# Optimization experiments

Hardware: AMD Instinct MI355X
Metric: run time of the kernel (lower is better)

## Reference

```python
import jax, jax.numpy as jnp
import numpy as np

D_MODEL = 1024
N_HEADS = 16
D_HEAD = D_MODEL // N_HEADS


def setup_inputs() -> dict:
    key = jax.random.key(0)
    k_x, k_qkv, k_out = jax.random.split(key, 3)
    x = jax.random.normal(k_x, (2, 2048, D_MODEL), dtype=jnp.float32)
    # nn.Linear weights: out = x @ W.T ; store as [out_features, in_features]
    s = 1.0 / np.sqrt(D_MODEL)
    w_qkv = jax.random.uniform(k_qkv, (3 * D_MODEL, D_MODEL), jnp.float32, -s, s)
    w_out = jax.random.uniform(k_out, (D_MODEL, D_MODEL), jnp.float32, -s, s)
    return {"x": x, "w_qkv": w_qkv, "w_out": w_out}


def reference(x, w_qkv, w_out):
    B, T, D = x.shape
    qkv = jnp.einsum("btd,ed->bte", x, w_qkv)  # [B,T,3D]
    q, k, v = jnp.split(qkv, 3, axis=-1)

    def heads(t):  # [B,T,D] -> [B,H,T,d]
        return t.reshape(B, T, N_HEADS, D_HEAD).transpose(0, 2, 1, 3)

    q, k, v = heads(q), heads(k), heads(v)
    scale = jnp.float32(np.sqrt(D_HEAD))
    scores = jnp.einsum("bhqd,bhkd->bhqk", q, k) / scale  # [B,H,T,T]
    causal = jnp.tril(jnp.ones((T, T), dtype=bool))  # True = keep
    scores = jnp.where(causal, scores, -jnp.inf)
    attn = jax.nn.softmax(scores, axis=-1)
    out = jnp.einsum("bhqk,bhkd->bhqd", attn, v)
    out = out.transpose(0, 2, 1, 3).reshape(B, T, D)
    return jnp.einsum("btd,ed->bte", out, w_out)
```

## Files before the change

### kernel.cpp

```cpp
#include <hip/hip_runtime.h>
#include <hip/hip_bf16.h>

typedef __attribute__((ext_vector_type(8))) short bf16x8;
typedef __attribute__((ext_vector_type(8))) unsigned short ushort8;
typedef __attribute__((ext_vector_type(4))) float f32x4;
typedef __attribute__((ext_vector_type(16))) float f32x16;

typedef const __attribute__((address_space(1))) void gvoid;
typedef __attribute__((address_space(3))) void svoid;

__device__ __forceinline__ unsigned short f2bf(float f) {
  union { float f; unsigned int u; } v; v.f = f;
  unsigned int u = v.u;
  unsigned int r = (u + 0x7fffu + ((u >> 16) & 1u)) >> 16;
  return (unsigned short)r;
}

__global__ void cast3_kernel(const float* __restrict__ a, int na4,
                             const float* __restrict__ b, int nb4,
                             const float* __restrict__ c, int nc4,
                             unsigned short* __restrict__ oa,
                             unsigned short* __restrict__ ob,
                             unsigned short* __restrict__ oc) {
  const int total = na4 + nb4 + nc4;
  for (int i = blockIdx.x * 256 + threadIdx.x; i < total; i += gridDim.x * 256) {
    const float* src; unsigned short* dst; int j = i;
    if (j < na4) { src = a; dst = oa; }
    else if (j < na4 + nb4) { j -= na4; src = b; dst = ob; }
    else { j -= na4 + nb4; src = c; dst = oc; }
    const float4 v = reinterpret_cast<const float4*>(src)[j];
    ushort4 o4;
    o4.x = f2bf(v.x); o4.y = f2bf(v.y); o4.z = f2bf(v.z); o4.w = f2bf(v.w);
    reinterpret_cast<ushort4*>(dst)[j] = o4;
  }
}

template<bool OUT_BF16>
__global__ __launch_bounds__(256) void gemm_bt(const unsigned short* __restrict__ A,
                                               const unsigned short* __restrict__ B,
                                               void* __restrict__ Cv,
                                               int M, int N, int K,
                                               float qscale, int qcols) {
  constexpr int BM = 128, BK = 32, TILE = BM * BK;
  __shared__ alignas(16) unsigned short As[2 * TILE];
  __shared__ alignas(16) unsigned short Bs[2 * TILE];
  const int tid = threadIdx.x;
  const int l  = tid & 63;
  const int w  = tid >> 6;
  const int wr = w >> 1, wc = w & 1;
  const int lr = l & 15, lg = l >> 4;
  const long tile_m = (long)blockIdx.x * BM;
  const long tile_n = (long)blockIdx.y * BM;

  const int c0 = tid, c1 = tid + 256;
  const unsigned short* pa0 = A + (tile_m + (c0 >> 2)) * (long)K + (c0 & 3) * 8;
  const unsigned short* pa1 = A + (tile_m + (c1 >> 2)) * (long)K + (c1 & 3) * 8;
  const unsigned short* pb0 = B + (tile_n + (c0 >> 2)) * (long)K + (c0 & 3) * 8;
  const unsigned short* pb1 = B + (tile_n + (c1 >> 2)) * (long)K + (c1 & 3) * 8;
  const int woff = w * 512;

  f32x4 acc[4][4] = {};

  __builtin_amdgcn_global_load_lds((gvoid*)pa0, (svoid*)(As + woff), 16, 0, 0);
  __builtin_amdgcn_global_load_lds((gvoid*)pa1, (svoid*)(As + 2048 + woff), 16, 0, 0);
  __builtin_amdgcn_global_load_lds((gvoid*)pb0, (svoid*)(Bs + woff), 16, 0, 0);
  __builtin_amdgcn_global_load_lds((gvoid*)pb1, (svoid*)(Bs + 2048 + woff), 16, 0, 0);
  __syncthreads();

  int cur = 0;
  for (int k0 = 0; k0 < K; k0 += BK) {
    if (k0 + BK < K) {
      unsigned short* An = As + (cur ^ 1) * TILE;
      unsigned short* Bn = Bs + (cur ^ 1) * TILE;
      __builtin_amdgcn_global_load_lds((gvoid*)(pa0 + k0 + BK), (svoid*)(An + woff), 16, 0, 0);
      __builtin_amdgcn_global_load_lds((gvoid*)(pa1 + k0 + BK), (svoid*)(An + 2048 + woff), 16, 0, 0);
      __builtin_amdgcn_global_load_lds((gvoid*)(pb0 + k0 + BK), (svoid*)(Bn + woff), 16, 0, 0);
      __builtin_amdgcn_global_load_lds((gvoid*)(pb1 + k0 + BK), (svoid*)(Bn + 2048 + woff), 16, 0, 0);
    }
    const unsigned short* AsC = As + cur * TILE;
    const unsigned short* BsC = Bs + cur * TILE;
    bf16x8 af[4], bfr[4];
#pragma unroll
    for (int m = 0; m < 4; ++m)
      af[m] = *reinterpret_cast<const bf16x8*>(AsC + (wr * 64 + m * 16 + lr) * BK + lg * 8);
#pragma unroll
    for (int n = 0; n < 4; ++n)
      bfr[n] = *reinterpret_cast<const bf16x8*>(BsC + (wc * 64 + n * 16 + lr) * BK + lg * 8);
#pragma unroll
    for (int m = 0; m < 4; ++m)
#pragma unroll
      for (int n = 0; n < 4; ++n)
        acc[m][n] = __builtin_amdgcn_mfma_f32_16x16x32_bf16(af[m], bfr[n], acc[m][n], 0, 0, 0);
    __syncthreads();
    cur ^= 1;
  }

#pragma unroll
  for (int m = 0; m < 4; ++m)
#pragma unroll
    for (int n = 0; n < 4; ++n)
#pragma unroll
      for (int r = 0; r < 4; ++r) {
        long row = tile_m + wr * 64 + m * 16 + lg * 4 + r;
        long col = tile_n + wc * 64 + n * 16 + lr;
        float sc = (col < qcols) ? qscale : 1.0f;
        if (OUT_BF16)
          reinterpret_cast<unsigned short*>(Cv)[row * N + col] = f2bf(acc[m][n][r] * sc);
        else
          reinterpret_cast<float*>(Cv)[row * N + col] = acc[m][n][r] * sc;
      }
}

__global__ __launch_bounds__(256, 2) void attn_kernel(const unsigned short* __restrict__ qkv,
                                                      unsigned short* __restrict__ o) {
  constexpr int E = 3072, T = 2048;
  __shared__ alignas(16) unsigned short Ks[64 * 64];
  __shared__ alignas(16) unsigned short Vt[64 * 64];
  __shared__ float alBuf[4][32];
  const int tid = threadIdx.x;
  const int l = tid & 63, w = tid >> 6;
  const int hh = l >> 5;
  const int lc = l & 31;
  const int id = blockIdx.x;
  const int half = id >> 8, rr2 = id & 255;
  const int bx = rr2 & 15;
  const int bh = (rr2 >> 4) | (half << 4);
  const int qtb = half ? (15 - bx) : bx;
  const int b = bh >> 4, hd = bh & 15;
  const unsigned short* Qb = qkv + (size_t)b * T * E + hd * 64;
  const unsigned short* Kb = Qb + 1024;
  const unsigned short* Vb = Qb + 2048;

  const int qrow0 = qtb * 128 + w * 32;
  const int qg = qrow0 + lc;
  const int nt = 2 * qtb + 2;

  const int kr0 = tid >> 3, js0 = tid & 7;
  const int kr1 = kr0 + 32;
  const unsigned short* sK = Kb + (size_t)kr0 * E + js0 * 8;
  const unsigned short* sV = Vb + (size_t)kr0 * E + js0 * 8;
  const size_t tileStep = (size_t)64 * E;

  bf16x8 aq[4];
#pragma unroll
  for (int c = 0; c < 4; ++c)
    aq[c] = *reinterpret_cast<const bf16x8*>(Qb + (size_t)qg * E + c * 16 + hh * 8);

  f32x16 accO0 = {}, accO1 = {};
  float mL = -1e30f, ls = 0.f;

  ushort8 k0 = *reinterpret_cast<const ushort8*>(sK);
  ushort8 k1 = *reinterpret_cast<const ushort8*>(sK + 32 * E);
  ushort8 v0 = *reinterpret_cast<const ushort8*>(sV);
  ushort8 v1 = *reinterpret_cast<const ushort8*>(sV + 32 * E);

  for (int t = 0; t < nt; ++t) {
    __syncthreads();
    *reinterpret_cast<ushort8*>(Ks + kr0 * 64 + ((js0 ^ (kr0 & 7)) << 3)) = k0;
    *reinterpret_cast<ushort8*>(Ks + kr1 * 64 + ((js0 ^ (kr1 & 7)) << 3)) = k1;
#pragma unroll
    for (int e = 0; e < 8; ++e) {
      int d = js0 * 8 + e;
      int swz = (d ^ (d >> 3)) & 7;
      Vt[d * 64 + ((((kr0 >> 3) ^ swz) << 3) | (kr0 & 7))] = (unsigned short)v0[e];
      Vt[d * 64 + ((((kr1 >> 3) ^ swz) << 3) | (kr1 & 7))] = (unsigned short)v1[e];
    }
    __syncthreads();
    if (t + 1 < nt) {
      const unsigned short* nK = sK + (size_t)(t + 1) * tileStep;
      const unsigned short* nV = sV + (size_t)(t + 1) * tileStep;
      k0 = *reinterpret_cast<const ushort8*>(nK);
      k1 = *reinterpret_cast<const ushort8*>(nK + 32 * E);
      v0 = *reinterpret_cast<const ushort8*>(nV);
      v1 = *reinterpret_cast<const ushort8*>(nV + 32 * E);
    }

    if (t * 64 > qrow0 + 31) continue;

    f32x16 sT0 = {}, sT1 = {};
#pragma unroll
    for (int c = 0; c < 4; ++c) {
      int sl = ((2 * c + hh) ^ (lc & 7)) << 3;
      bf16x8 ak0 = *reinterpret_cast<const bf16x8*>(Ks + lc * 64 + sl);
      bf16x8 ak1 = *reinterpret_cast<const bf16x8*>(Ks + (32 + lc) * 64 + sl);
      sT0 = __builtin_amdgcn_mfma_f32_32x32x16_bf16(ak0, aq[c], sT0, 0, 0, 0);
      sT1 = __builtin_amdgcn_mfma_f32_32x32x16_bf16(ak1, aq[c], sT1, 0, 0, 0);
    }

    const bool needMask = (t * 64 + 63) > qrow0;
    float pm = -1e30f;
#pragma unroll
    for (int r = 0; r < 16; ++r) {
      int kb = t * 64 + (r & 3) + 8 * (r >> 2) + 4 * hh;
      float a0 = sT0[r], a1 = sT1[r];
      if (needMask) {
        if (kb > qg) a0 = -1e30f;
        if (kb + 32 > qg) a1 = -1e30f;
      }
      sT0[r] = a0; sT1[r] = a1;
      pm = fmaxf(pm, fmaxf(a0, a1));
    }
    pm = fmaxf(pm, __shfl_xor(pm, 32));

    if (__any(pm > mL + 8.f)) {
      float mn = fmaxf(mL, pm);
      float al = __expf(mL - mn);
      mL = mn;
      ls *= al;
      alBuf[w][lc] = al;
      asm volatile("s_waitcnt lgkmcnt(0)" ::: "memory");
      __builtin_amdgcn_sched_barrier(0);
#pragma unroll
      for (int r = 0; r < 16; ++r) {
        float alr = alBuf[w][(r & 3) + 8 * (r >> 2) + 4 * hh];
        accO0[r] *= alr;
        accO1[r] *= alr;
      }
    }

    bf16x8 pa[4];
    union U4 { unsigned int u[4]; bf16x8 v; };
#pragma unroll
    for (int n = 0; n < 2; ++n) {
      float p[16];
#pragma unroll
      for (int r = 0; r < 16; ++r) {
        float pv = __expf((n ? sT1[r] : sT0[r]) - mL);
        p[r] = pv;
        ls += pv;
      }
#pragma unroll
      for (int gg = 0; gg < 2; ++gg) {
        unsigned int x0, x1, y0, y1;
        asm("v_cvt_pk_bf16_f32 %0, %1, %2" : "=v"(x0) : "v"(p[8 * gg + 0]), "v"(p[8 * gg + 1]));
        asm("v_cvt_pk_bf16_f32 %0, %1, %2" : "=v"(x1) : "v"(p[8 * gg + 2]), "v"(p[8 * gg + 3]));
        asm("v_cvt_pk_bf16_f32 %0, %1, %2" : "=v"(y0) : "v"(p[8 * gg + 4]), "v"(p[8 * gg + 5]));
        asm("v_cvt_pk_bf16_f32 %0, %1, %2" : "=v"(y1) : "v"(p[8 * gg + 6]), "v"(p[8 * gg + 7]));
        asm("v_permlane32_swap_b32 %0, %1" : "+v"(x0), "+v"(y0));
        asm("v_permlane32_swap_b32 %0, %1" : "+v"(x1), "+v"(y1));
        U4 fu;
        fu.u[0] = x0; fu.u[1] = x1; fu.u[2] = y0; fu.u[3] = y1;
        pa[2 * n + gg] = fu.v;
      }
    }

#pragma unroll
    for (int cp = 0; cp < 4; ++cp) {
      int d0 = lc, d1 = 32 + lc;
      int sl0 = ((2 * cp + hh) ^ ((d0 ^ (d0 >> 3)) & 7)) << 3;
      int sl1 = ((2 * cp + hh) ^ ((d1 ^ (d1 >> 3)) & 7)) << 3;
      bf16x8 bv0 = *reinterpret_cast<const bf16x8*>(Vt + d0 * 64 + sl0);
      bf16x8 bv1 = *reinterpret_cast<const bf16x8*>(Vt + d1 * 64 + sl1);
      accO0 = __builtin_amdgcn_mfma_f32_32x32x16_bf16(pa[cp], bv0, accO0, 0, 0, 0);
      accO1 = __builtin_amdgcn_mfma_f32_32x32x16_bf16(pa[cp], bv1, accO1, 0, 0, 0);
    }
  }

  float inv = 1.f / (ls + __shfl_xor(ls, 32));
  alBuf[w][lc] = inv;
  asm volatile("s_waitcnt lgkmcnt(0)" ::: "memory");
  __builtin_amdgcn_sched_barrier(0);
#pragma unroll
  for (int r = 0; r < 16; ++r) {
    int q = (r & 3) + 8 * (r >> 2) + 4 * hh;
    float iv = alBuf[w][q];
    size_t row = (size_t)(b * T + qrow0 + q) * 1024 + hd * 64;
    o[row + lc]      = f2bf(accO0[r] * iv);
    o[row + 32 + lc] = f2bf(accO1[r] * iv);
  }
}

extern "C" void kernel_launch(void* const* d_in, const int* in_sizes, int n_in,
                              void* d_out, int out_size, void* d_ws, size_t ws_size,
                              hipStream_t stream) {
  const float* x     = (const float*)d_in[0];
  const float* w_qkv = (const float*)d_in[1];
  const float* w_out = (const float*)d_in[2];
  float* out = (float*)d_out;

  unsigned short* xb    = (unsigned short*)d_ws;
  unsigned short* wqkvb = xb    + (size_t)4096 * 1024;
  unsigned short* woutb = wqkvb + (size_t)3072 * 1024;
  unsigned short* qkv   = woutb + (size_t)1024 * 1024;
  unsigned short* attn  = qkv   + (size_t)4096 * 3072;

  cast3_kernel<<<dim3(2048), 256, 0, stream>>>(x,     4096 * 1024 / 4,
                                               w_qkv, 3072 * 1024 / 4,
                                               w_out, 1024 * 1024 / 4,
                                               xb, wqkvb, woutb);

  gemm_bt<true ><<<dim3(32, 24), 256, 0, stream>>>(xb,   wqkvb, (void*)qkv,  4096, 3072, 1024,
                                                   0.125f, 1024);
  attn_kernel  <<<dim3(512), 256, 0, stream>>>(qkv, attn);
  gemm_bt<false><<<dim3(32,  8), 256, 0, stream>>>(attn, woutb, (void*)out, 4096, 1024, 1024,
                                                   1.0f, 0);
}
```

Baseline: 116.8 us.

## Split attention key tiles across two wave groups and merge softmax partials

The attention block grows to 512 threads. Each pair of waves shares the same 32 query rows, and each wave handles one 32-key half of every 64-key tile with its own running max and sum. At the end the two partial outputs are combined through shared memory with a log-sum-exp rescale. This aims to double the waves per block so more latency can be hidden, and it halves per-wave score work and register pressure. In exchange it adds shared memory for the merge, an extra reduction phase, and a larger workgroup that may fit fewer blocks per CU.

```diff
diff --git a/kernel.cpp b/kernel.cpp
--- a/kernel.cpp
+++ b/kernel.cpp
@@ -111,16 +111,20 @@
       }
 }
 
-__global__ __launch_bounds__(256, 2) void attn_kernel(const unsigned short* __restrict__ qkv,
+__global__ __launch_bounds__(512, 2) void attn_kernel(const unsigned short* __restrict__ qkv,
                                                       unsigned short* __restrict__ o) {
   constexpr int E = 3072, T = 2048;
   __shared__ alignas(16) unsigned short Ks[64 * 64];
   __shared__ alignas(16) unsigned short Vt[64 * 64];
-  __shared__ float alBuf[4][32];
+  __shared__ float OB[4][32][64];
+  __shared__ float alBuf[8][32];
+  __shared__ float mB[4][32], lB[4][32], fA[4][32], fB[4][32];
   const int tid = threadIdx.x;
   const int l = tid & 63, w = tid >> 6;
   const int hh = l >> 5;
   const int lc = l & 31;
+  const int wq = w & 3;
+  const int h2 = w >> 2;
   const int id = blockIdx.x;
   const int half = id >> 8, rr2 = id & 255;
   const int bx = rr2 & 15;
@@ -131,14 +135,13 @@
   const unsigned short* Kb = Qb + 1024;
   const unsigned short* Vb = Qb + 2048;
 
-  const int qrow0 = qtb * 128 + w * 32;
+  const int qrow0 = qtb * 128 + wq * 32;
   const int qg = qrow0 + lc;
   const int nt = 2 * qtb + 2;
 
-  const int kr0 = tid >> 3, js0 = tid & 7;
-  const int kr1 = kr0 + 32;
-  const unsigned short* sK = Kb + (size_t)kr0 * E + js0 * 8;
-  const unsigned short* sV = Vb + (size_t)kr0 * E + js0 * 8;
+  const int kr = tid >> 3, js = tid & 7;
+  const unsigned short* sK = Kb + (size_t)kr * E + js * 8;
+  const unsigned short* sV = Vb + (size_t)kr * E + js * 8;
   const size_t tileStep = (size_t)64 * E;
 
   bf16x8 aq[4];
@@ -150,55 +153,43 @@
   float mL = -1e30f, ls = 0.f;
 
   ushort8 k0 = *reinterpret_cast<const ushort8*>(sK);
-  ushort8 k1 = *reinterpret_cast<const ushort8*>(sK + 32 * E);
   ushort8 v0 = *reinterpret_cast<const ushort8*>(sV);
-  ushort8 v1 = *reinterpret_cast<const ushort8*>(sV + 32 * E);
+  const int ksl = (js ^ (kr & 7)) << 3;
 
   for (int t = 0; t < nt; ++t) {
     __syncthreads();
-    *reinterpret_cast<ushort8*>(Ks + kr0 * 64 + ((js0 ^ (kr0 & 7)) << 3)) = k0;
-    *reinterpret_cast<ushort8*>(Ks + kr1 * 64 + ((js0 ^ (kr1 & 7)) << 3)) = k1;
+    *reinterpret_cast<ushort8*>(Ks + kr * 64 + ksl) = k0;
 #pragma unroll
     for (int e = 0; e < 8; ++e) {
-      int d = js0 * 8 + e;
+      int d = js * 8 + e;
       int swz = (d ^ (d >> 3)) & 7;
-      Vt[d * 64 + ((((kr0 >> 3) ^ swz) << 3) | (kr0 & 7))] = (unsigned short)v0[e];
-      Vt[d * 64 + ((((kr1 >> 3) ^ swz) << 3) | (kr1 & 7))] = (unsigned short)v1[e];
+      Vt[d * 64 + ((((kr >> 3) ^ swz) << 3) | (kr & 7))] = (unsigned short)v0[e];
     }
     __syncthreads();
     if (t + 1 < nt) {
-      const unsigned short* nK = sK + (size_t)(t + 1) * tileStep;
-      const unsigned short* nV = sV + (size_t)(t + 1) * tileStep;
-      k0 = *reinterpret_cast<const ushort8*>(nK);
-      k1 = *reinterpret_cast<const ushort8*>(nK + 32 * E);
-      v0 = *reinterpret_cast<const ushort8*>(nV);
-      v1 = *reinterpret_cast<const ushort8*>(nV + 32 * E);
-    }
-
-    if (t * 64 > qrow0 + 31) continue;
-
-    f32x16 sT0 = {}, sT1 = {};
+      k0 = *reinterpret_cast<const ushort8*>(sK + (size_t)(t + 1) * tileStep);
+      v0 = *reinterpret_cast<const ushort8*>(sV + (size_t)(t + 1) * tileStep);
+    }
+
+    if (t * 64 + 32 * h2 > qrow0 + 31) continue;
+
+    f32x16 sT0 = {};
 #pragma unroll
     for (int c = 0; c < 4; ++c) {
       int sl = ((2 * c + hh) ^ (lc & 7)) << 3;
-      bf16x8 ak0 = *reinterpret_cast<const bf16x8*>(Ks + lc * 64 + sl);
-      bf16x8 ak1 = *reinterpret_cast<const bf16x8*>(Ks + (32 + lc) * 64 + sl);
+      bf16x8 ak0 = *reinterpret_cast<const bf16x8*>(Ks + (32 * h2 + lc) * 64 + sl);
       sT0 = __builtin_amdgcn_mfma_f32_32x32x16_bf16(ak0, aq[c], sT0, 0, 0, 0);
-      sT1 = __builtin_amdgcn_mfma_f32_32x32x16_bf16(ak1, aq[c], sT1, 0, 0, 0);
-    }
-
-    const bool needMask = (t * 64 + 63) > qrow0;
+    }
+
+    const bool needMask = (t * 64 + 32 * h2 + 31) > qrow0;
     float pm = -1e30f;
 #pragma unroll
     for (int r = 0; r < 16; ++r) {
-      int kb = t * 64 + (r & 3) + 8 * (r >> 2) + 4 * hh;
-      float a0 = sT0[r], a1 = sT1[r];
-      if (needMask) {
-        if (kb > qg) a0 = -1e30f;
-        if (kb + 32 > qg) a1 = -1e30f;
-      }
-      sT0[r] = a0; sT1[r] = a1;
-      pm = fmaxf(pm, fmaxf(a0, a1));
+      int kb = t * 64 + 32 * h2 + (r & 3) + 8 * (r >> 2) + 4 * hh;
+      float a0 = sT0[r];
+      if (needMask && kb > qg) a0 = -1e30f;
+      sT0[r] = a0;
+      pm = fmaxf(pm, a0);
     }
     pm = fmaxf(pm, __shfl_xor(pm, 32));
 
@@ -218,14 +209,13 @@
       }
     }
 
-    bf16x8 pa[4];
+    bf16x8 pa0, pa1;
     union U4 { unsigned int u[4]; bf16x8 v; };
-#pragma unroll
-    for (int n = 0; n < 2; ++n) {
+    {
       float p[16];
 #pragma unroll
       for (int r = 0; r < 16; ++r) {
-        float pv = __expf((n ? sT1[r] : sT0[r]) - mL);
+        float pv = __expf(sT0[r] - mL);
         p[r] = pv;
         ls += pv;
       }
@@ -240,33 +230,55 @@
         asm("v_permlane32_swap_b32 %0, %1" : "+v"(x1), "+v"(y1));
         U4 fu;
         fu.u[0] = x0; fu.u[1] = x1; fu.u[2] = y0; fu.u[3] = y1;
-        pa[2 * n + gg] = fu.v;
+        if (gg == 0) pa0 = fu.v; else pa1 = fu.v;
       }
     }
 
 #pragma unroll
-    for (int cp = 0; cp < 4; ++cp) {
+    for (int gg = 0; gg < 2; ++gg) {
+      int cp = 2 * h2 + gg;
+      bf16x8 ap = gg ? pa1 : pa0;
       int d0 = lc, d1 = 32 + lc;
       int sl0 = ((2 * cp + hh) ^ ((d0 ^ (d0 >> 3)) & 7)) << 3;
       int sl1 = ((2 * cp + hh) ^ ((d1 ^ (d1 >> 3)) & 7)) << 3;
       bf16x8 bv0 = *reinterpret_cast<const bf16x8*>(Vt + d0 * 64 + sl0);
       bf16x8 bv1 = *reinterpret_cast<const bf16x8*>(Vt + d1 * 64 + sl1);
-      accO0 = __builtin_amdgcn_mfma_f32_32x32x16_bf16(pa[cp], bv0, accO0, 0, 0, 0);
-      accO1 = __builtin_amdgcn_mfma_f32_32x32x16_bf16(pa[cp], bv1, accO1, 0, 0, 0);
-    }
-  }
-
-  float inv = 1.f / (ls + __shfl_xor(ls, 32));
-  alBuf[w][lc] = inv;
-  asm volatile("s_waitcnt lgkmcnt(0)" ::: "memory");
-  __builtin_amdgcn_sched_barrier(0);
-#pragma unroll
-  for (int r = 0; r < 16; ++r) {
-    int q = (r & 3) + 8 * (r >> 2) + 4 * hh;
-    float iv = alBuf[w][q];
-    size_t row = (size_t)(b * T + qrow0 + q) * 1024 + hd * 64;
-    o[row + lc]      = f2bf(accO0[r] * iv);
-    o[row + 32 + lc] = f2bf(accO1[r] * iv);
+      accO0 = __builtin_amdgcn_mfma_f32_32x32x16_bf16(ap, bv0, accO0, 0, 0, 0);
+      accO1 = __builtin_amdgcn_mfma_f32_32x32x16_bf16(ap, bv1, accO1, 0, 0, 0);
+    }
+  }
+
+  float lsT = ls + __shfl_xor(ls, 32);
+  __syncthreads();
+  if (h2 == 1) {
+    if (hh == 0) { mB[wq][lc] = mL; lB[wq][lc] = lsT; }
+#pragma unroll
+    for (int r = 0; r < 16; ++r) {
+      int q = (r & 3) + 8 * (r >> 2) + 4 * hh;
+      OB[wq][q][lc]      = accO0[r];
+      OB[wq][q][32 + lc] = accO1[r];
+    }
+  }
+  __syncthreads();
+  if (h2 == 0) {
+    float mO = mB[wq][lc], lO = lB[wq][lc];
+    float mS = fmaxf(mL, mO);
+    float eA = __expf(mL - mS), eB = __expf(mO - mS);
+    float inv = 1.f / (lsT * eA + lO * eB);
+    fA[wq][lc] = eA * inv;
+    fB[wq][lc] = eB * inv;
+    asm volatile("s_waitcnt lgkmcnt(0)" ::: "memory");
+    __builtin_amdgcn_sched_barrier(0);
+#pragma unroll
+    for (int r = 0; r < 16; ++r) {
+      int q = (r & 3) + 8 * (r >> 2) + 4 * hh;
+      float a = fA[wq][q], bb = fB[wq][q];
+      float o0 = accO0[r] * a + OB[wq][q][lc] * bb;
+      float o1 = accO1[r] * a + OB[wq][q][32 + lc] * bb;
+      size_t row = (size_t)(b * T + qrow0 + q) * 1024 + hd * 64;
+      o[row + lc]      = f2bf(o0);
+      o[row + 32 + lc] = f2bf(o1);
+    }
   }
 }
 
@@ -291,7 +303,7 @@
 
   gemm_bt<true ><<<dim3(32, 24), 256, 0, stream>>>(xb,   wqkvb, (void*)qkv,  4096, 3072, 1024,
                                                    0.125f, 1024);
-  attn_kernel  <<<dim3(512), 256, 0, stream>>>(qkv, attn);
+  attn_kernel  <<<dim3(512), 512, 0, stream>>>(qkv, attn);
   gemm_bt<false><<<dim3(32,  8), 256, 0, stream>>>(attn, woutb, (void*)out, 4096, 1024, 1024,
                                                    1.0f, 0);
 }
```

Measured after the change: 125.5 us. 7.5% more time.

## Split long causal query tiles across two blocks and merge partial softmax results

Applied to the files above, without the earlier changes.

Query tiles 8-15 of the causal attention are split along the key dimension into two blocks each, with a static table that balances work per block and orders the heavy jobs first. The split blocks write unnormalized bf16 partial outputs plus their row max and row sum into workspace reused from the x and w_qkv cast buffers. A new merge kernel then rescales and combines the two partials. The aim is better load balance and fuller CU occupancy across 768 blocks, at the cost of an extra launch, extra global traffic, and bf16 rounding of the partial sums.

```diff
diff --git a/kernel.cpp b/kernel.cpp
--- a/kernel.cpp
+++ b/kernel.cpp
@@ -14,6 +14,9 @@
   unsigned int u = v.u;
   unsigned int r = (u + 0x7fffu + ((u >> 16) & 1u)) >> 16;
   return (unsigned short)r;
+}
+__device__ __forceinline__ float bf2f(unsigned short u) {
+  union { unsigned int i; float f; } v; v.i = ((unsigned int)u) << 16; return v.f;
 }
 
 __global__ void cast3_kernel(const float* __restrict__ a, int na4,
@@ -112,20 +115,30 @@
 }
 
 __global__ __launch_bounds__(256, 2) void attn_kernel(const unsigned short* __restrict__ qkv,
-                                                      unsigned short* __restrict__ o) {
+                                                      unsigned short* __restrict__ o,
+                                                      unsigned short* __restrict__ Opart,
+                                                      float* __restrict__ mpart,
+                                                      float* __restrict__ lpart) {
   constexpr int E = 3072, T = 2048;
   __shared__ alignas(16) unsigned short Ks[64 * 64];
   __shared__ alignas(16) unsigned short Vt[64 * 64];
   __shared__ float alBuf[4][32];
+
+  static const int jq[24]  = {15,15, 7,14,14,13,13, 6,12,12,11,11, 5,10,10, 9, 9, 4, 8, 8, 3, 2, 1, 0};
+  static const int jt0[24] = { 0,16, 0, 0,15, 0,14, 0, 0,13, 0,12, 0, 0,11, 0,10, 0, 0, 9, 0, 0, 0, 0};
+  static const int jt1[24] = {16,32,16,15,30,14,28,14,13,26,12,24,12,11,22,10,20,10, 9,18, 8, 6, 4, 2};
+
   const int tid = threadIdx.x;
   const int l = tid & 63, w = tid >> 6;
   const int hh = l >> 5;
   const int lc = l & 31;
-  const int id = blockIdx.x;
-  const int half = id >> 8, rr2 = id & 255;
-  const int bx = rr2 & 15;
-  const int bh = (rr2 >> 4) | (half << 4);
-  const int qtb = half ? (15 - bx) : bx;
+  int jj = blockIdx.x >> 5;
+  if (jj >= 8 && jj < 16) jj = 23 - jj;
+  const int bh = blockIdx.x & 31;
+  const int qtb = jq[jj], t0 = jt0[jj], t1 = jt1[jj];
+  const bool isSplit = (qtb >= 8);
+  const int part = (t0 != 0) ? 1 : 0;
+  const int pidx = (((bh << 3) + (qtb - 8)) << 1) + part;
   const int b = bh >> 4, hd = bh & 15;
   const unsigned short* Qb = qkv + (size_t)b * T * E + hd * 64;
   const unsigned short* Kb = Qb + 1024;
@@ -133,7 +146,6 @@
 
   const int qrow0 = qtb * 128 + w * 32;
   const int qg = qrow0 + lc;
-  const int nt = 2 * qtb + 2;
 
   const int kr0 = tid >> 3, js0 = tid & 7;
   const int kr1 = kr0 + 32;
@@ -149,12 +161,12 @@
   f32x16 accO0 = {}, accO1 = {};
   float mL = -1e30f, ls = 0.f;
 
-  ushort8 k0 = *reinterpret_cast<const ushort8*>(sK);
-  ushort8 k1 = *reinterpret_cast<const ushort8*>(sK + 32 * E);
-  ushort8 v0 = *reinterpret_cast<const ushort8*>(sV);
-  ushort8 v1 = *reinterpret_cast<const ushort8*>(sV + 32 * E);
-
-  for (int t = 0; t < nt; ++t) {
+  ushort8 k0 = *reinterpret_cast<const ushort8*>(sK + (size_t)t0 * tileStep);
+  ushort8 k1 = *reinterpret_cast<const ushort8*>(sK + (size_t)t0 * tileStep + 32 * E);
+  ushort8 v0 = *reinterpret_cast<const ushort8*>(sV + (size_t)t0 * tileStep);
+  ushort8 v1 = *reinterpret_cast<const ushort8*>(sV + (size_t)t0 * tileStep + 32 * E);
+
+  for (int t = t0; t < t1; ++t) {
     __syncthreads();
     *reinterpret_cast<ushort8*>(Ks + kr0 * 64 + ((js0 ^ (kr0 & 7)) << 3)) = k0;
     *reinterpret_cast<ushort8*>(Ks + kr1 * 64 + ((js0 ^ (kr1 & 7)) << 3)) = k1;
@@ -166,7 +178,7 @@
       Vt[d * 64 + ((((kr1 >> 3) ^ swz) << 3) | (kr1 & 7))] = (unsigned short)v1[e];
     }
     __syncthreads();
-    if (t + 1 < nt) {
+    if (t + 1 < t1) {
       const unsigned short* nK = sK + (size_t)(t + 1) * tileStep;
       const unsigned short* nV = sV + (size_t)(t + 1) * tileStep;
       k0 = *reinterpret_cast<const ushort8*>(nK);
@@ -256,18 +268,59 @@
     }
   }
 
-  float inv = 1.f / (ls + __shfl_xor(ls, 32));
-  alBuf[w][lc] = inv;
-  asm volatile("s_waitcnt lgkmcnt(0)" ::: "memory");
-  __builtin_amdgcn_sched_barrier(0);
-#pragma unroll
-  for (int r = 0; r < 16; ++r) {
-    int q = (r & 3) + 8 * (r >> 2) + 4 * hh;
-    float iv = alBuf[w][q];
-    size_t row = (size_t)(b * T + qrow0 + q) * 1024 + hd * 64;
-    o[row + lc]      = f2bf(accO0[r] * iv);
-    o[row + 32 + lc] = f2bf(accO1[r] * iv);
+  float lsT = ls + __shfl_xor(ls, 32);
+  if (isSplit) {
+    if (hh == 0) {
+      mpart[pidx * 128 + w * 32 + lc] = mL;
+      lpart[pidx * 128 + w * 32 + lc] = lsT;
+    }
+#pragma unroll
+    for (int r = 0; r < 16; ++r) {
+      int q = (r & 3) + 8 * (r >> 2) + 4 * hh;
+      int rp = w * 32 + q;
+      Opart[(size_t)pidx * 8192 + rp * 64 + lc]      = f2bf(accO0[r]);
+      Opart[(size_t)pidx * 8192 + rp * 64 + 32 + lc] = f2bf(accO1[r]);
+    }
+  } else {
+    float inv = 1.f / lsT;
+    alBuf[w][lc] = inv;
+    asm volatile("s_waitcnt lgkmcnt(0)" ::: "memory");
+    __builtin_amdgcn_sched_barrier(0);
+#pragma unroll
+    for (int r = 0; r < 16; ++r) {
+      int q = (r & 3) + 8 * (r >> 2) + 4 * hh;
+      float iv = alBuf[w][q];
+      size_t row = (size_t)(b * T + qrow0 + q) * 1024 + hd * 64;
+      o[row + lc]      = f2bf(accO0[r] * iv);
+      o[row + 32 + lc] = f2bf(accO1[r] * iv);
+    }
   }
+}
+
+__global__ __launch_bounds__(256) void merge_kernel(const unsigned short* __restrict__ Opart,
+                                                    const float* __restrict__ mpart,
+                                                    const float* __restrict__ lpart,
+                                                    unsigned short* __restrict__ o) {
+  const int e = blockIdx.x * 256 + threadIdx.x;
+  const int rowid = e >> 3, c8 = e & 7;
+  const int bh = rowid >> 10, rem = rowid & 1023;
+  const int q8 = rem >> 7, r = rem & 127;
+  const int b = bh >> 4, hd = bh & 15;
+  const int p0 = (((bh << 3) + q8) << 1);
+  const float m0 = mpart[p0 * 128 + r], m1 = mpart[(p0 + 1) * 128 + r];
+  const float l0 = lpart[p0 * 128 + r], l1 = lpart[(p0 + 1) * 128 + r];
+  const float mS = fmaxf(m0, m1);
+  const float e0 = __expf(m0 - mS), e1 = __expf(m1 - mS);
+  const float inv = 1.f / (l0 * e0 + l1 * e1);
+  const float f0 = e0 * inv, f1 = e1 * inv;
+  const ushort8 a = *reinterpret_cast<const ushort8*>(Opart + (size_t)p0 * 8192 + r * 64 + c8 * 8);
+  const ushort8 bb = *reinterpret_cast<const ushort8*>(Opart + (size_t)(p0 + 1) * 8192 + r * 64 + c8 * 8);
+  ushort8 out;
+#pragma unroll
+  for (int j = 0; j < 8; ++j)
+    out[j] = f2bf(bf2f(a[j]) * f0 + bf2f(bb[j]) * f1);
+  const size_t row = (size_t)(b * 2048 + (q8 + 8) * 128 + r) * 1024 + hd * 64 + c8 * 8;
+  *reinterpret_cast<ushort8*>(o + row) = out;
 }
 
 extern "C" void kernel_launch(void* const* d_in, const int* in_sizes, int n_in,
@@ -284,6 +337,10 @@
   unsigned short* qkv   = woutb + (size_t)1024 * 1024;
   unsigned short* attn  = qkv   + (size_t)4096 * 3072;
 
+  unsigned short* Opart = xb;
+  float* mpart = (float*)wqkvb;
+  float* lpart = mpart + 512 * 128;
+
   cast3_kernel<<<dim3(2048), 256, 0, stream>>>(x,     4096 * 1024 / 4,
                                                w_qkv, 3072 * 1024 / 4,
                                                w_out, 1024 * 1024 / 4,
@@ -291,7 +348,8 @@
 
   gemm_bt<true ><<<dim3(32, 24), 256, 0, stream>>>(xb,   wqkvb, (void*)qkv,  4096, 3072, 1024,
                                                    0.125f, 1024);
-  attn_kernel  <<<dim3(512), 256, 0, stream>>>(qkv, attn);
+  attn_kernel  <<<dim3(768), 256, 0, stream>>>(qkv, attn, Opart, mpart, lpart);
+  merge_kernel <<<dim3(1024), 256, 0, stream>>>(Opart, mpart, lpart, attn);
   gemm_bt<false><<<dim3(32,  8), 256, 0, stream>>>(attn, woutb, (void*)out, 4096, 1024, 1024,
                                                    1.0f, 0);
 }
```

New measurement: 108.3 us. 7.2% less time.
